# Optimization experiments

Measured on AMD Instinct MI355X. Metric: run time of the kernel, lower is better.

## Reference

```python
import jax, jax.numpy as jnp
import numpy as np


def setup_inputs() -> dict:
    key = jax.random.key(0)
    kq, kk, kv = jax.random.split(key, 3)
    N, T, F = 16, 2048, 128
    q = jax.random.normal(kq, (N, T, F), dtype=jnp.float32)
    k = jax.random.normal(kk, (N, T, F), dtype=jnp.float32)
    v = jax.random.normal(kv, (N, T, F), dtype=jnp.float32)
    return {"q": q, "k": k, "v": v, "masked": 1}


def reference(q, k, v, masked):
    # scores: [N, T, T] = q @ k^T / sqrt(F)
    F = q.shape[-1]
    scores = jnp.einsum("ntf,nsf->nts", q, k) / jnp.sqrt(jnp.asarray(F, q.dtype))
    if masked:
        T = q.shape[1]
        causal = jnp.tril(jnp.ones((T, T), dtype=bool))  # [T, T]
        scores = jnp.where(causal[None, :, :], scores, jnp.asarray(-1e9, scores.dtype))
    attn = jax.nn.softmax(scores, axis=-1)
    # dropout is identity in eval/reference mode
    return jnp.einsum("nts,nsf->ntf", attn, v)
```

## Files before the change

kernel.cpp:

```cpp
#include <hip/hip_runtime.h>
#include <hip/hip_bf16.h>
#include <stdint.h>

#define T_SEQ 2048
#define DH    128
#define BKV   64
#define QSCALE 0.12751742796f
#define SLOT_F 16640
#define WS_NEEDED 55115776ULL

typedef short  short8 __attribute__((ext_vector_type(8)));
typedef __bf16 bf16x8 __attribute__((ext_vector_type(8)));
typedef float  f32x4  __attribute__((ext_vector_type(4)));

__device__ __forceinline__ bf16x8 as_bf16x8(short8 x) { return __builtin_bit_cast(bf16x8, x); }

__device__ __forceinline__ uint32_t bf_bits(float x) {
  union { __hip_bfloat16 h; unsigned short u; } cv;
  cv.h = __float2bfloat16(x);
  return (uint32_t)cv.u;
}

__global__ void prep_kv(const float* __restrict__ k, const float* __restrict__ v,
                        unsigned short* __restrict__ kb, unsigned short* __restrict__ vt) {
  __shared__ float tile[64][65];
  const int n = blockIdx.y, x = blockIdx.x, tid = threadIdx.x;
  if (x < 256) {
    const int i = (n * 256 + x) * 256 + tid;
    const float4 f = ((const float4*)k)[i];
    union { unsigned short us[4]; uint2 u2; } o;
    o.us[0] = (unsigned short)bf_bits(f.x);
    o.us[1] = (unsigned short)bf_bits(f.y);
    o.us[2] = (unsigned short)bf_bits(f.z);
    o.us[3] = (unsigned short)bf_bits(f.w);
    ((uint2*)kb)[i] = o.u2;
  } else {
    const int x2 = x - 256;
    const int t0 = (x2 & 31) * 64, d0 = (x2 >> 5) * 64;
    const int tx = tid & 63, ty = tid >> 6;
    #pragma unroll
    for (int i = 0; i < 64; i += 4)
      tile[ty + i][tx] = v[((size_t)n * T_SEQ + t0 + ty + i) * DH + d0 + tx];
    __syncthreads();
    const int sig = 32 * (tx >> 5) + 16 * ((tx >> 2) & 1) + 4 * ((tx >> 3) & 3) + (tx & 3);
    #pragma unroll
    for (int i = 0; i < 64; i += 4)
      vt[((size_t)n * DH + d0 + ty + i) * T_SEQ + t0 + tx] = (unsigned short)bf_bits(tile[sig][ty + i]);
  }
}

__global__ __launch_bounds__(512, 4) void attn_fwd(
    const float* __restrict__ Qf,
    const unsigned short* __restrict__ Kb,
    const unsigned short* __restrict__ Vt,
    float* __restrict__ Out,
    float* __restrict__ Part,
    const int* __restrict__ maskp,
    int use_split)
{
  __shared__ __align__(16) char smem[65536];

  const int tid  = threadIdx.x;
  const int lane = tid & 63;
  const int w    = tid >> 6;
  const int m15  = lane & 15;
  const int g    = lane >> 4;

  const int bid = blockIdx.x;
  const int n   = (bid & 7) + 8 * ((bid >> 3) & 1);
  const int job = bid >> 4;
  const int masked = maskp[0];

  int Q, c, k0, k1, nc;
  if (masked && use_split) {
    int base = 0; Q = 0;
    for (;;) { int ncq = (2 * Q + 9) >> 3; if (job < base + ncq) { c = job - base; break; } base += ncq; ++Q; }
    nc = (2 * Q + 9) >> 3;
    k0 = c * 8;
    k1 = min(k0 + 8, 2 * Q + 2);
  } else {
    if (job >= 16) return;
    Q = job; c = 0; nc = 1; k0 = 0;
    k1 = masked ? (2 * Q + 2) : (T_SEQ / BKV);
  }

  const int qrow = Q * 128 + 16 * w + m15;

  bf16x8 qf[4];
  {
    const float* qg = Qf + ((size_t)n * T_SEQ + qrow) * DH;
    #pragma unroll
    for (int kf = 0; kf < 4; ++kf) {
      const float4 f0 = *(const float4*)(qg + 32 * kf + 8 * g);
      const float4 f1 = *(const float4*)(qg + 32 * kf + 8 * g + 4);
      union { unsigned short us[8]; short8 s8; } qa;
      qa.us[0] = (unsigned short)bf_bits(f0.x * QSCALE);
      qa.us[1] = (unsigned short)bf_bits(f0.y * QSCALE);
      qa.us[2] = (unsigned short)bf_bits(f0.z * QSCALE);
      qa.us[3] = (unsigned short)bf_bits(f0.w * QSCALE);
      qa.us[4] = (unsigned short)bf_bits(f1.x * QSCALE);
      qa.us[5] = (unsigned short)bf_bits(f1.y * QSCALE);
      qa.us[6] = (unsigned short)bf_bits(f1.z * QSCALE);
      qa.us[7] = (unsigned short)bf_bits(f1.w * QSCALE);
      qf[kf] = as_bf16x8(qa.s8);
    }
  }

  f32x4 acc[8] = {};
  float m_run = -3.0e38f;
  float ssum  = 0.f;
  const int swz = (m15 & 7) << 4;

  short8 kreg[2], vreg[2];
  const short8* gK = (const short8*)(Kb + (size_t)n * T_SEQ * DH);
  const short8* gV = (const short8*)(Vt + (size_t)n * DH * T_SEQ);

  auto loadRegs = [&](int kt) {
    const int t0 = kt * BKV;
    #pragma unroll
    for (int i = 0; i < 2; ++i) {
      int row = 8 * w + 4 * i + g;
      kreg[i] = gK[(size_t)(t0 + row) * 16 + m15];
    }
    #pragma unroll
    for (int i = 0; i < 2; ++i) {
      int d = 16 * w + 8 * i + (lane >> 3);
      vreg[i] = gV[(size_t)d * 256 + (t0 >> 3) + (lane & 7)];
    }
  };
  auto writeRegs = [&](int buf) {
    #pragma unroll
    for (int i = 0; i < 2; ++i) {
      int row = 8 * w + 4 * i + g;
      int off = buf * 16384 + row * 256 + ((m15 * 16) ^ ((row & 7) << 4));
      *(short8*)(smem + off) = kreg[i];
    }
    #pragma unroll
    for (int i = 0; i < 2; ++i) {
      int d = 16 * w + 8 * i + (lane >> 3);
      int off = 32768 + buf * 16384 + d * 128 + (((lane & 7) * 16) ^ ((d & 7) << 4));
      *(short8*)(smem + off) = vreg[i];
    }
  };

  loadRegs(k0);
  writeRegs(k0 & 1);

  for (int kt = k0; kt < k1; ++kt) {
    __syncthreads();
    if (kt + 1 < k1) loadRegs(kt + 1);

    const char* kb = smem + (kt & 1) * 16384;
    const char* vb = smem + 32768 + (kt & 1) * 16384;

    f32x4 s[4] = {};
    __builtin_amdgcn_s_setprio(1);
    #pragma unroll
    for (int kf = 0; kf < 4; ++kf) {
      #pragma unroll
      for (int ma = 0; ma < 4; ++ma) {
        short8 kfr = *(const short8*)(kb + (16 * ma + m15) * 256 + ((g * 16 + 64 * kf) ^ swz));
        s[ma] = __builtin_amdgcn_mfma_f32_16x16x32_bf16(as_bf16x8(kfr), qf[kf], s[ma], 0, 0, 0);
      }
    }
    __builtin_amdgcn_s_setprio(0);

    if (masked && kt >= 2 * Q) {
      #pragma unroll
      for (int ma = 0; ma < 4; ++ma)
        #pragma unroll
        for (int rr = 0; rr < 4; ++rr) {
          int kvg = kt * BKV + ma * 16 + g * 4 + rr;
          if (kvg > qrow) s[ma][rr] = -1.0e30f;
        }
    }

    float mx = s[0][0];
    #pragma unroll
    for (int ma = 0; ma < 4; ++ma)
      #pragma unroll
      for (int rr = 0; rr < 4; ++rr) mx = fmaxf(mx, s[ma][rr]);
    mx = fmaxf(mx, __shfl_xor(mx, 16));
    mx = fmaxf(mx, __shfl_xor(mx, 32));

    if (!__all(mx <= m_run + 8.0f)) {
      float mnew = fmaxf(m_run, mx);
      float corr = exp2f(m_run - mnew);
      ssum *= corr;
      #pragma unroll
      for (int i = 0; i < 8; ++i) {
        acc[i][0] *= corr; acc[i][1] *= corr; acc[i][2] *= corr; acc[i][3] *= corr;
      }
      m_run = mnew;
    }

    float p[4][4];
    float lsum = 0.f;
    #pragma unroll
    for (int ma = 0; ma < 4; ++ma)
      #pragma unroll
      for (int rr = 0; rr < 4; ++rr) { p[ma][rr] = exp2f(s[ma][rr] - m_run); lsum += p[ma][rr]; }
    lsum += __shfl_xor(lsum, 16);
    lsum += __shfl_xor(lsum, 32);
    ssum += lsum;

    uint32_t u[4][2];
    #pragma unroll
    for (int ma = 0; ma < 4; ++ma) {
      u[ma][0] = bf_bits(p[ma][0]) | (bf_bits(p[ma][1]) << 16);
      u[ma][1] = bf_bits(p[ma][2]) | (bf_bits(p[ma][3]) << 16);
    }

    bf16x8 pfr[2];
    #pragma unroll
    for (int ks = 0; ks < 2; ++ks) {
      union { uint32_t q[4]; short8 s8; } pu;
      pu.q[0] = u[2 * ks + 0][0];
      pu.q[1] = u[2 * ks + 0][1];
      pu.q[2] = u[2 * ks + 1][0];
      pu.q[3] = u[2 * ks + 1][1];
      pfr[ks] = as_bf16x8(pu.s8);
    }

    __builtin_amdgcn_s_setprio(1);
    #pragma unroll
    for (int dsub = 0; dsub < 8; ++dsub) {
      #pragma unroll
      for (int ks = 0; ks < 2; ++ks) {
        short8 vfr = *(const short8*)(vb + (16 * dsub + m15) * 128 + ((g * 16 + 64 * ks) ^ swz));
        acc[dsub] = __builtin_amdgcn_mfma_f32_16x16x32_bf16(as_bf16x8(vfr), pfr[ks], acc[dsub], 0, 0, 0);
      }
    }
    __builtin_amdgcn_s_setprio(0);

    if (kt + 1 < k1) writeRegs((kt + 1) & 1);
  }

  if (nc == 1) {
    const float inv = 1.0f / ssum;
    float* ob = Out + ((size_t)n * T_SEQ + qrow) * DH;
    #pragma unroll
    for (int dsub = 0; dsub < 8; ++dsub) {
      f32x4 o;
      o[0] = acc[dsub][0] * inv; o[1] = acc[dsub][1] * inv;
      o[2] = acc[dsub][2] * inv; o[3] = acc[dsub][3] * inv;
      *(f32x4*)(ob + dsub * 16 + g * 4) = o;
    }
  } else {
    int b8 = 0;
    for (int qq = 4; qq < Q; ++qq) b8 += (2 * qq + 9) >> 3;
    float* slot = Part + ((size_t)n * 36 + b8 + c) * SLOT_F;
    const int qr = 16 * w + m15;
    if (g == 0) { slot[qr] = m_run; slot[128 + qr] = ssum; }
    float* so = slot + 256 + (size_t)qr * 128;
    #pragma unroll
    for (int dsub = 0; dsub < 8; ++dsub)
      *(f32x4*)(so + dsub * 16 + 4 * g) = acc[dsub];
  }
}

__global__ void combine_kernel(const float* __restrict__ Part, float* __restrict__ Out,
                               const int* __restrict__ maskp, int use_split) {
  if (!maskp[0] || !use_split) return;
  const int cb = blockIdx.x;
  const int n  = cb & 15;
  const int Q  = (cb >> 4) + 4;
  const int nc = (2 * Q + 9) >> 3;
  int b8 = 0;
  for (int qq = 4; qq < Q; ++qq) b8 += (2 * qq + 9) >> 3;
  const float* slot0 = Part + ((size_t)n * 36 + b8) * SLOT_F;

  const int tid = threadIdx.x;
  const int q   = tid >> 1;
  const int d0  = (tid & 1) * 64;

  float m[4], s[4], wgt[4];
  float M = -3.0e38f;
  for (int i = 0; i < nc; ++i) {
    m[i] = slot0[(size_t)i * SLOT_F + q];
    s[i] = slot0[(size_t)i * SLOT_F + 128 + q];
    M = fmaxf(M, m[i]);
  }
  float denom = 0.f;
  for (int i = 0; i < nc; ++i) { wgt[i] = exp2f(m[i] - M); denom += s[i] * wgt[i]; }
  const float inv = 1.0f / denom;

  float* ob = Out + ((size_t)n * T_SEQ + Q * 128 + q) * DH + d0;
  #pragma unroll
  for (int j = 0; j < 16; ++j) {
    f32x4 a = {};
    for (int i = 0; i < nc; ++i) {
      const f32x4 v = *(const f32x4*)(slot0 + (size_t)i * SLOT_F + 256 + (size_t)q * 128 + d0 + 4 * j);
      a[0] += v[0] * wgt[i]; a[1] += v[1] * wgt[i]; a[2] += v[2] * wgt[i]; a[3] += v[3] * wgt[i];
    }
    a[0] *= inv; a[1] *= inv; a[2] *= inv; a[3] *= inv;
    *(f32x4*)(ob + 4 * j) = a;
  }
}

extern "C" void kernel_launch(void* const* d_in, const int* in_sizes, int n_in,
                              void* d_out, int out_size, void* d_ws, size_t ws_size,
                              hipStream_t stream) {
  (void)in_sizes; (void)n_in; (void)out_size;
  const float* q = (const float*)d_in[0];
  const float* k = (const float*)d_in[1];
  const float* v = (const float*)d_in[2];
  const int* maskp = (const int*)d_in[3];
  float* out = (float*)d_out;

  const size_t elems = (size_t)16 * T_SEQ * DH;
  unsigned short* Kb = (unsigned short*)d_ws;
  unsigned short* Vt = Kb + elems;
  float* Part = (float*)d_ws + elems;
  const int use_split = (ws_size >= WS_NEEDED) ? 1 : 0;

  prep_kv<<<dim3(320, 16), 256, 0, stream>>>(k, v, Kb, Vt);
  attn_fwd<<<dim3(640), 512, 0, stream>>>(q, Kb, Vt, out, Part, maskp, use_split);
  combine_kernel<<<dim3(192), 256, 0, stream>>>(Part, out, maskp, use_split);
}
```

Measured before the change: 156.1 us.

## Process two 16-row query subtiles per wave, halving block threads

```diff
diff --git a/kernel.cpp b/kernel.cpp
--- a/kernel.cpp
+++ b/kernel.cpp
@@ -49,7 +49,7 @@
   }
 }
 
-__global__ __launch_bounds__(512, 4) void attn_fwd(
+__global__ __launch_bounds__(256, 2) void attn_fwd(
     const float* __restrict__ Qf,
     const unsigned short* __restrict__ Kb,
     const unsigned short* __restrict__ Vt,
@@ -84,11 +84,12 @@
     k1 = masked ? (2 * Q + 2) : (T_SEQ / BKV);
   }
 
-  const int qrow = Q * 128 + 16 * w + m15;
-
-  bf16x8 qf[4];
-  {
-    const float* qg = Qf + ((size_t)n * T_SEQ + qrow) * DH;
+  const int qrow0 = Q * 128 + 32 * w + m15;
+
+  bf16x8 qf[2][4];
+  #pragma unroll
+  for (int sub = 0; sub < 2; ++sub) {
+    const float* qg = Qf + ((size_t)n * T_SEQ + qrow0 + 16 * sub) * DH;
     #pragma unroll
     for (int kf = 0; kf < 4; ++kf) {
       const float4 f0 = *(const float4*)(qg + 32 * kf + 8 * g);
@@ -102,42 +103,42 @@
       qa.us[5] = (unsigned short)bf_bits(f1.y * QSCALE);
       qa.us[6] = (unsigned short)bf_bits(f1.z * QSCALE);
       qa.us[7] = (unsigned short)bf_bits(f1.w * QSCALE);
-      qf[kf] = as_bf16x8(qa.s8);
-    }
-  }
-
-  f32x4 acc[8] = {};
-  float m_run = -3.0e38f;
-  float ssum  = 0.f;
+      qf[sub][kf] = as_bf16x8(qa.s8);
+    }
+  }
+
+  f32x4 acc[2][8] = {};
+  float m_run[2] = {-3.0e38f, -3.0e38f};
+  float ssum[2]  = {0.f, 0.f};
   const int swz = (m15 & 7) << 4;
 
-  short8 kreg[2], vreg[2];
+  short8 kreg[4], vreg[4];
   const short8* gK = (const short8*)(Kb + (size_t)n * T_SEQ * DH);
   const short8* gV = (const short8*)(Vt + (size_t)n * DH * T_SEQ);
 
   auto loadRegs = [&](int kt) {
     const int t0 = kt * BKV;
     #pragma unroll
-    for (int i = 0; i < 2; ++i) {
-      int row = 8 * w + 4 * i + g;
+    for (int i = 0; i < 4; ++i) {
+      int row = 16 * w + 4 * i + g;
       kreg[i] = gK[(size_t)(t0 + row) * 16 + m15];
     }
     #pragma unroll
-    for (int i = 0; i < 2; ++i) {
-      int d = 16 * w + 8 * i + (lane >> 3);
+    for (int i = 0; i < 4; ++i) {
+      int d = 32 * w + 8 * i + (lane >> 3);
       vreg[i] = gV[(size_t)d * 256 + (t0 >> 3) + (lane & 7)];
     }
   };
   auto writeRegs = [&](int buf) {
     #pragma unroll
-    for (int i = 0; i < 2; ++i) {
-      int row = 8 * w + 4 * i + g;
+    for (int i = 0; i < 4; ++i) {
+      int row = 16 * w + 4 * i + g;
       int off = buf * 16384 + row * 256 + ((m15 * 16) ^ ((row & 7) << 4));
       *(short8*)(smem + off) = kreg[i];
     }
     #pragma unroll
-    for (int i = 0; i < 2; ++i) {
-      int d = 16 * w + 8 * i + (lane >> 3);
+    for (int i = 0; i < 4; ++i) {
+      int d = 32 * w + 8 * i + (lane >> 3);
       int off = 32768 + buf * 16384 + d * 128 + (((lane & 7) * 16) ^ ((d & 7) << 4));
       *(short8*)(smem + off) = vreg[i];
     }
@@ -153,73 +154,80 @@
     const char* kb = smem + (kt & 1) * 16384;
     const char* vb = smem + 32768 + (kt & 1) * 16384;
 
-    f32x4 s[4] = {};
+    f32x4 s[2][4] = {};
     __builtin_amdgcn_s_setprio(1);
     #pragma unroll
     for (int kf = 0; kf < 4; ++kf) {
       #pragma unroll
       for (int ma = 0; ma < 4; ++ma) {
         short8 kfr = *(const short8*)(kb + (16 * ma + m15) * 256 + ((g * 16 + 64 * kf) ^ swz));
-        s[ma] = __builtin_amdgcn_mfma_f32_16x16x32_bf16(as_bf16x8(kfr), qf[kf], s[ma], 0, 0, 0);
+        s[0][ma] = __builtin_amdgcn_mfma_f32_16x16x32_bf16(as_bf16x8(kfr), qf[0][kf], s[0][ma], 0, 0, 0);
+        s[1][ma] = __builtin_amdgcn_mfma_f32_16x16x32_bf16(as_bf16x8(kfr), qf[1][kf], s[1][ma], 0, 0, 0);
       }
     }
     __builtin_amdgcn_s_setprio(0);
 
     if (masked && kt >= 2 * Q) {
+      #pragma unroll
+      for (int sub = 0; sub < 2; ++sub)
+        #pragma unroll
+        for (int ma = 0; ma < 4; ++ma)
+          #pragma unroll
+          for (int rr = 0; rr < 4; ++rr) {
+            int kvg = kt * BKV + ma * 16 + g * 4 + rr;
+            if (kvg > qrow0 + 16 * sub) s[sub][ma][rr] = -1.0e30f;
+          }
+    }
+
+    float mx[2];
+    #pragma unroll
+    for (int sub = 0; sub < 2; ++sub) {
+      float m = s[sub][0][0];
       #pragma unroll
       for (int ma = 0; ma < 4; ++ma)
         #pragma unroll
-        for (int rr = 0; rr < 4; ++rr) {
-          int kvg = kt * BKV + ma * 16 + g * 4 + rr;
-          if (kvg > qrow) s[ma][rr] = -1.0e30f;
+        for (int rr = 0; rr < 4; ++rr) m = fmaxf(m, s[sub][ma][rr]);
+      m = fmaxf(m, __shfl_xor(m, 16));
+      m = fmaxf(m, __shfl_xor(m, 32));
+      mx[sub] = m;
+    }
+
+    if (!__all(mx[0] <= m_run[0] + 8.0f && mx[1] <= m_run[1] + 8.0f)) {
+      #pragma unroll
+      for (int sub = 0; sub < 2; ++sub) {
+        float mnew = fmaxf(m_run[sub], mx[sub]);
+        float corr = exp2f(m_run[sub] - mnew);
+        ssum[sub] *= corr;
+        #pragma unroll
+        for (int i = 0; i < 8; ++i) {
+          acc[sub][i][0] *= corr; acc[sub][i][1] *= corr;
+          acc[sub][i][2] *= corr; acc[sub][i][3] *= corr;
         }
-    }
-
-    float mx = s[0][0];
-    #pragma unroll
-    for (int ma = 0; ma < 4; ++ma)
-      #pragma unroll
-      for (int rr = 0; rr < 4; ++rr) mx = fmaxf(mx, s[ma][rr]);
-    mx = fmaxf(mx, __shfl_xor(mx, 16));
-    mx = fmaxf(mx, __shfl_xor(mx, 32));
-
-    if (!__all(mx <= m_run + 8.0f)) {
-      float mnew = fmaxf(m_run, mx);
-      float corr = exp2f(m_run - mnew);
-      ssum *= corr;
-      #pragma unroll
-      for (int i = 0; i < 8; ++i) {
-        acc[i][0] *= corr; acc[i][1] *= corr; acc[i][2] *= corr; acc[i][3] *= corr;
-      }
-      m_run = mnew;
-    }
-
-    float p[4][4];
-    float lsum = 0.f;
-    #pragma unroll
-    for (int ma = 0; ma < 4; ++ma)
-      #pragma unroll
-      for (int rr = 0; rr < 4; ++rr) { p[ma][rr] = exp2f(s[ma][rr] - m_run); lsum += p[ma][rr]; }
-    lsum += __shfl_xor(lsum, 16);
-    lsum += __shfl_xor(lsum, 32);
-    ssum += lsum;
-
-    uint32_t u[4][2];
-    #pragma unroll
-    for (int ma = 0; ma < 4; ++ma) {
-      u[ma][0] = bf_bits(p[ma][0]) | (bf_bits(p[ma][1]) << 16);
-      u[ma][1] = bf_bits(p[ma][2]) | (bf_bits(p[ma][3]) << 16);
-    }
-
-    bf16x8 pfr[2];
-    #pragma unroll
-    for (int ks = 0; ks < 2; ++ks) {
-      union { uint32_t q[4]; short8 s8; } pu;
-      pu.q[0] = u[2 * ks + 0][0];
-      pu.q[1] = u[2 * ks + 0][1];
-      pu.q[2] = u[2 * ks + 1][0];
-      pu.q[3] = u[2 * ks + 1][1];
-      pfr[ks] = as_bf16x8(pu.s8);
+        m_run[sub] = mnew;
+      }
+    }
+
+    bf16x8 pfr[2][2];
+    #pragma unroll
+    for (int sub = 0; sub < 2; ++sub) {
+      float p[4][4];
+      float lsum = 0.f;
+      #pragma unroll
+      for (int ma = 0; ma < 4; ++ma)
+        #pragma unroll
+        for (int rr = 0; rr < 4; ++rr) { p[ma][rr] = exp2f(s[sub][ma][rr] - m_run[sub]); lsum += p[ma][rr]; }
+      lsum += __shfl_xor(lsum, 16);
+      lsum += __shfl_xor(lsum, 32);
+      ssum[sub] += lsum;
+      #pragma unroll
+      for (int ks = 0; ks < 2; ++ks) {
+        union { uint32_t q[4]; short8 s8; } pu;
+        pu.q[0] = bf_bits(p[2 * ks + 0][0]) | (bf_bits(p[2 * ks + 0][1]) << 16);
+        pu.q[1] = bf_bits(p[2 * ks + 0][2]) | (bf_bits(p[2 * ks + 0][3]) << 16);
+        pu.q[2] = bf_bits(p[2 * ks + 1][0]) | (bf_bits(p[2 * ks + 1][1]) << 16);
+        pu.q[3] = bf_bits(p[2 * ks + 1][2]) | (bf_bits(p[2 * ks + 1][3]) << 16);
+        pfr[sub][ks] = as_bf16x8(pu.s8);
+      }
     }
 
     __builtin_amdgcn_s_setprio(1);
@@ -228,7 +236,8 @@
       #pragma unroll
       for (int ks = 0; ks < 2; ++ks) {
         short8 vfr = *(const short8*)(vb + (16 * dsub + m15) * 128 + ((g * 16 + 64 * ks) ^ swz));
-        acc[dsub] = __builtin_amdgcn_mfma_f32_16x16x32_bf16(as_bf16x8(vfr), pfr[ks], acc[dsub], 0, 0, 0);
+        acc[0][dsub] = __builtin_amdgcn_mfma_f32_16x16x32_bf16(as_bf16x8(vfr), pfr[0][ks], acc[0][dsub], 0, 0, 0);
+        acc[1][dsub] = __builtin_amdgcn_mfma_f32_16x16x32_bf16(as_bf16x8(vfr), pfr[1][ks], acc[1][dsub], 0, 0, 0);
       }
     }
     __builtin_amdgcn_s_setprio(0);
@@ -237,25 +246,31 @@
   }
 
   if (nc == 1) {
-    const float inv = 1.0f / ssum;
-    float* ob = Out + ((size_t)n * T_SEQ + qrow) * DH;
-    #pragma unroll
-    for (int dsub = 0; dsub < 8; ++dsub) {
-      f32x4 o;
-      o[0] = acc[dsub][0] * inv; o[1] = acc[dsub][1] * inv;
-      o[2] = acc[dsub][2] * inv; o[3] = acc[dsub][3] * inv;
-      *(f32x4*)(ob + dsub * 16 + g * 4) = o;
+    #pragma unroll
+    for (int sub = 0; sub < 2; ++sub) {
+      const float inv = 1.0f / ssum[sub];
+      float* ob = Out + ((size_t)n * T_SEQ + qrow0 + 16 * sub) * DH;
+      #pragma unroll
+      for (int dsub = 0; dsub < 8; ++dsub) {
+        f32x4 o;
+        o[0] = acc[sub][dsub][0] * inv; o[1] = acc[sub][dsub][1] * inv;
+        o[2] = acc[sub][dsub][2] * inv; o[3] = acc[sub][dsub][3] * inv;
+        *(f32x4*)(ob + dsub * 16 + g * 4) = o;
+      }
     }
   } else {
     int b8 = 0;
     for (int qq = 4; qq < Q; ++qq) b8 += (2 * qq + 9) >> 3;
     float* slot = Part + ((size_t)n * 36 + b8 + c) * SLOT_F;
-    const int qr = 16 * w + m15;
-    if (g == 0) { slot[qr] = m_run; slot[128 + qr] = ssum; }
-    float* so = slot + 256 + (size_t)qr * 128;
-    #pragma unroll
-    for (int dsub = 0; dsub < 8; ++dsub)
-      *(f32x4*)(so + dsub * 16 + 4 * g) = acc[dsub];
+    #pragma unroll
+    for (int sub = 0; sub < 2; ++sub) {
+      const int qr = 32 * w + 16 * sub + m15;
+      if (g == 0) { slot[qr] = m_run[sub]; slot[128 + qr] = ssum[sub]; }
+      float* so = slot + 256 + (size_t)qr * 128;
+      #pragma unroll
+      for (int dsub = 0; dsub < 8; ++dsub)
+        *(f32x4*)(so + dsub * 16 + 4 * g) = acc[sub][dsub];
+    }
   }
 }
 
@@ -315,6 +330,6 @@
   const int use_split = (ws_size >= WS_NEEDED) ? 1 : 0;
 
   prep_kv<<<dim3(320, 16), 256, 0, stream>>>(k, v, Kb, Vt);
-  attn_fwd<<<dim3(640), 512, 0, stream>>>(q, Kb, Vt, out, Part, maskp, use_split);
+  attn_fwd<<<dim3(640), 256, 0, stream>>>(q, Kb, Vt, out, Part, maskp, use_split);
   combine_kernel<<<dim3(192), 256, 0, stream>>>(Part, out, maskp, use_split);
 }
```

Measured after the change: 158.9 us. About the same (+1.8%).
